# Kernel tuning notes

Hardware: AMD Instinct MI355X
Metric: run time of the kernel (lower is better)

The kernel has to match this reference:

```python
import jax, jax.numpy as jnp
import numpy as np

B, CH, N = 131072, 2, 8  # batch, pos/neg channels, coarse graph size
L1, L2 = 64, 32          # latent_gcn, latent2_gcn
NEG_SLOPE = 0.2


def _row_normalize(a):
    # GCN-style row normalization: D^-1 A, zeroing rows with zero sum
    rowsum = a.sum(-1, keepdims=True)
    r_inv = jnp.where(rowsum > 0, 1.0 / rowsum, 0.0)
    return a * r_inv


def _leaky(x):
    return jnp.where(x >= 0, x, NEG_SLOPE * x)


def setup_inputs() -> dict:
    key = jax.random.key(0)
    ks = jax.random.split(key, 16)
    u = lambda k, shape, s: jax.random.uniform(k, shape, jnp.float32, -s, s)
    s1 = 1.0 / np.sqrt(L1)
    s2 = 1.0 / np.sqrt(L2)
    d_in = CH * N * L2            # 512
    d_h1 = N * N                  # 64
    d_h2 = int(N * N * 0.5)       # 32
    return {
        "adj": jax.random.uniform(ks[0], (B, CH, N, N), jnp.float32),
        "Wp1": u(ks[1], (N, L1), s1),  "bp1": u(ks[2], (L1,), s1),
        "Wp2": u(ks[3], (L1, L2), s2), "bp2": u(ks[4], (L2,), s2),
        "Wn1": u(ks[5], (N, L1), s1),  "bn1": u(ks[6], (L1,), s1),
        "Wn2": u(ks[7], (L1, L2), s2), "bn2": u(ks[8], (L2,), s2),
        "Wl1": u(ks[9], (d_in, d_h1), 1.0 / np.sqrt(d_in)),  "bl1": u(ks[10], (d_h1,), 1.0 / np.sqrt(d_in)),
        "Wl2": u(ks[11], (d_h1, d_h2), 1.0 / np.sqrt(d_h1)), "bl2": u(ks[12], (d_h2,), 1.0 / np.sqrt(d_h1)),
        "Wl3": u(ks[13], (d_h2, 1), 1.0 / np.sqrt(d_h2)),    "bl3": u(ks[14], (1,), 1.0 / np.sqrt(d_h2)),
    }


def reference(adj, Wp1, bp1, Wp2, bp2, Wn1, bn1, Wn2, bn2,
              Wl1, bl1, Wl2, bl2, Wl3, bl3):
    # adj: [B, 2, N, N]; channel 0 -> positive GCN, channel 1 -> negative GCN
    Ap = _row_normalize(adj[:, 0])  # [B, N, N]
    An = _row_normalize(adj[:, 1])

    # input features x = eye(N), so eye @ W == W; keep general via broadcast
    def gcn2(A, W1, b1, W2, b2):
        x1 = _leaky(jnp.einsum('bij,jk->bik', A, W1) + b1)        # [B, N, L1]
        x2 = _leaky(jnp.einsum('bij,bjk->bik', A, x1 @ W2) + b2)  # [B, N, L2]
        return x2

    xp = gcn2(Ap, Wp1, bp1, Wp2, bp2)
    xn = gcn2(An, Wn1, bn1, Wn2, bn2)
    x_ = jnp.stack([xp, xn], axis=1)          # [B, 2, N, L2]
    x = x_.reshape(x_.shape[0], -1)           # [B, 2*N*L2]

    h = _leaky(x @ Wl1 + bl1)
    h = _leaky(h @ Wl2 + bl2)
    return h @ Wl3 + bl3                      # [B, 1]
```

## Files before the change

kernel.cpp:

```cpp
#include <hip/hip_runtime.h>

typedef _Float16 f16;
typedef _Float16 f16x2 __attribute__((ext_vector_type(2)));
typedef _Float16 f16x4 __attribute__((ext_vector_type(4)));
typedef _Float16 f16x8 __attribute__((ext_vector_type(8)));
typedef float    f32x4 __attribute__((ext_vector_type(4)));
typedef unsigned int u32;
typedef u32      u32x2 __attribute__((ext_vector_type(2)));
typedef u32      u32x4 __attribute__((ext_vector_type(4)));

#define MFMA32(a, b, c) __builtin_amdgcn_mfma_f32_16x16x32_f16((a), (b), (c), 0, 0, 0)
#define MFMA16(a, b, c) __builtin_amdgcn_mfma_f32_16x16x16f16((a), (b), (c), 0, 0, 0)

#define TILES 8

__device__ __forceinline__ float leaky(float x) {
    return fmaf(0.4f, __builtin_fabsf(x), 0.6f * x);
}
__device__ __forceinline__ u32 pkrtz(float a, float b) {
    return __builtin_bit_cast(u32, __builtin_amdgcn_cvt_pkrtz(a, b));
}
__device__ __forceinline__ u32 lk_pk2(float a, float b) {
    f16x2 v = __builtin_bit_cast(f16x2, __builtin_amdgcn_cvt_pkrtz(a, b));
    f16x2 z2 = {(f16)0.0f, (f16)0.0f};
    f16x2 mx = __builtin_elementwise_max(v, z2);
    f16x2 mn = __builtin_elementwise_min(v, z2);
    f16x2 r = mn * (f16x2){(f16)0.2f, (f16)0.2f} + mx;
    return __builtin_bit_cast(u32, r);
}
__device__ __forceinline__ f16x4 lk_pk4(const f32x4 z) {
    return __builtin_bit_cast(f16x4, (u32x2){ lk_pk2(z[0], z[1]), lk_pk2(z[2], z[3]) });
}
__device__ __forceinline__ f16x4 pk4(const f32x4 z) {
    return __builtin_bit_cast(f16x4, (u32x2){ pkrtz(z[0], z[1]), pkrtz(z[2], z[3]) });
}
__device__ __forceinline__ void st_lk4(void* p, const f32x4 z) {
    *(u32x2*)p = (u32x2){ lk_pk2(z[0], z[1]), lk_pk2(z[2], z[3]) };
}

__global__ void disc_prepack(const float* __restrict__ Wp1, const float* __restrict__ Wp2,
                             const float* __restrict__ Wn1, const float* __restrict__ Wn2,
                             const float* __restrict__ Wl1, const float* __restrict__ Wl2,
                             f16* __restrict__ ws)
{
    int idx = blockIdx.x * 256 + threadIdx.x;
    if (idx >= 84 * 512 + 24 * 256) return;
    float v = 0.0f;
    if (idx < 84 * 512) {
        int f = idx >> 9, r = idx & 511;
        int lane = r >> 3, e = r & 7;
        int m15 = lane & 15, h = lane >> 4;
        if (f < 64) {
            int mt4 = f >> 4, ks4 = f & 15;
            int k = ks4 * 32 + h * 8 + e;
            v = Wl1[k * 64 + mt4 * 16 + m15];
        } else if (f < 72) {
            int q = f - 64, c = q >> 2, mt = q & 3;
            const float* W1 = c ? Wn1 : Wp1;
            v = (lane < 16) ? W1[e * 64 + mt * 16 + m15] : 0.0f;
        } else if (f < 80) {
            int q = f - 72, c = q >> 2, nt2 = (q >> 1) & 1, ks2 = q & 1;
            const float* W2 = c ? Wn2 : Wp2;
            int k = ks2 * 32 + h * 8 + e;
            v = W2[k * 32 + nt2 * 16 + m15];
        } else {
            int q = f - 80, ms5 = q >> 1, ks5 = q & 1;
            int k = ks5 * 32 + h * 8 + e;
            v = Wl2[k * 32 + ms5 * 16 + m15];
        }
    } else {
        int r2 = idx - 84 * 512;
        int f2 = r2 >> 8, rr = r2 & 255;
        int lane = rr >> 2, e = rr & 3;
        int m15 = lane & 15, h = lane >> 4;
        if (f2 < 16) {
            int c = f2 >> 3, kb = (f2 >> 1) & 3, nt = f2 & 1;
            const float* W2 = c ? Wn2 : Wp2;
            v = W2[(kb * 16 + h * 4 + e) * 32 + nt * 16 + m15];
        } else {
            int q = f2 - 16, kb = q >> 1, nt = q & 1;
            v = Wl2[(kb * 16 + h * 4 + e) * 32 + nt * 16 + m15];
        }
    }
    ws[idx] = (f16)v;
}

__global__ __launch_bounds__(128, 2) void disc_main(
    const float* __restrict__ adj,
    const float* __restrict__ bp1, const float* __restrict__ bp2,
    const float* __restrict__ bn1, const float* __restrict__ bn2,
    const float* __restrict__ bl1, const float* __restrict__ bl2,
    const float* __restrict__ bl3, const float* __restrict__ Wl3,
    const f16* __restrict__ ws, float* __restrict__ out)
{
    extern __shared__ char smem[];
    const int tid  = threadIdx.x;
    const int lane = tid & 63;
    const int wid  = tid >> 6;
    const int h    = lane >> 4;
    const int m15  = lane & 15;
    const int i7   = lane & 7;
    const int r8   = m15 >> 3;

    const f16x8* wsf = (const f16x8*)ws;
    const f16x4* wsq = (const f16x4*)(ws + 84 * 512);
    const int c = wid;

    const f16x8* w1p = wsf + (64 + c * 4) * 64 + lane;
    f16x8 w1t0 = w1p[0], w1t1 = w1p[64], w1t2 = w1p[128], w1t3 = w1p[192];
    const f16x4* w2p = wsq + (c * 8) * 64 + lane;
    f16x4 w2k00 = w2p[0],   w2k01 = w2p[64];
    f16x4 w2k10 = w2p[128], w2k11 = w2p[192];
    f16x4 w2k20 = w2p[256], w2k21 = w2p[320];
    f16x4 w2k30 = w2p[384], w2k31 = w2p[448];
    const f32x4* b1p = (const f32x4*)(c ? bn1 : bp1);
    f32x4 b10 = b1p[h], b11 = b1p[4 + h], b12 = b1p[8 + h], b13 = b1p[12 + h];
    const f32x4* b2p = (const f32x4*)(c ? bn2 : bp2);
    f32x4 b20 = b2p[h], b21 = b2p[4 + h];
    f32x4 bl1v0 = ((const f32x4*)bl1)[h],      bl1v1 = ((const f32x4*)bl1)[4 + h];
    f32x4 bl1v2 = ((const f32x4*)bl1)[8 + h],  bl1v3 = ((const f32x4*)bl1)[12 + h];

    f16x4 l200, l201, l210, l211, l220, l221, l230, l231;
    float c0 = 0.0f, c1 = 0.0f, w30 = 0.0f, w31 = 0.0f, bl3s = 0.0f;
    if (wid == 0) {
        const f16x4* wl2p = wsq + 16 * 64 + lane;
        l200 = wl2p[0];   l201 = wl2p[64];
        l210 = wl2p[128]; l211 = wl2p[192];
        l220 = wl2p[256]; l221 = wl2p[320];
        l230 = wl2p[384]; l231 = wl2p[448];
        c0 = bl2[m15]; c1 = bl2[m15 + 16];
        w30 = Wl3[m15]; w31 = Wl3[m15 + 16];
        bl3s = bl3[0];
    }

    char* wbase = smem + wid * 10240;
    char* Albuf = wbase;
    char* xbuf  = wbase + 2048;

    const int rxor = ((m15 >> 1) & 3) << 4;
    const bool bsel = ((h >> 1) == r8);
    const int  hlow = h & 1;
    f32x4 zero4 = {0.0f, 0.0f, 0.0f, 0.0f};
    f16x4 zf4 = {};

    long b0 = (long)blockIdx.x * (16 * TILES);

    f32x4 c00, c01, c10, c11;
    {
        const f32x4* rp0 = (const f32x4*)(adj + (b0 + (lane >> 3)) * 128 + c * 64 + (lane & 7) * 8);
        c00 = rp0[0]; c01 = rp0[1];
        const int rid1 = 64 + lane;
        const f32x4* rp1 = (const f32x4*)(adj + (b0 + (rid1 >> 3)) * 128 + c * 64 + (rid1 & 7) * 8);
        c10 = rp1[0]; c11 = rp1[1];
    }

    #pragma unroll 1
    for (int it = 0; it < TILES; ++it, b0 += 16) {
        {
            float s = ((c00[0] + c00[1]) + (c00[2] + c00[3])) + ((c01[0] + c01[1]) + (c01[2] + c01[3]));
            float rv = (s > 0.0f) ? __builtin_amdgcn_rcpf(s) : 0.0f;
            u32x4 row = { pkrtz(c00[0] * rv, c00[1] * rv), pkrtz(c00[2] * rv, c00[3] * rv),
                          pkrtz(c01[0] * rv, c01[1] * rv), pkrtz(c01[2] * rv, c01[3] * rv) };
            *(u32x4*)(Albuf + lane * 16) = row;
        }
        {
            float s = ((c10[0] + c10[1]) + (c10[2] + c10[3])) + ((c11[0] + c11[1]) + (c11[2] + c11[3]));
            float rv = (s > 0.0f) ? __builtin_amdgcn_rcpf(s) : 0.0f;
            u32x4 row = { pkrtz(c10[0] * rv, c10[1] * rv), pkrtz(c10[2] * rv, c10[3] * rv),
                          pkrtz(c11[0] * rv, c11[1] * rv), pkrtz(c11[2] * rv, c11[3] * rv) };
            *(u32x4*)(Albuf + (64 + lane) * 16) = row;
        }

        f32x4 n00, n01, n10, n11;
        const bool more = (it + 1 < TILES);
        if (more) {
            const f32x4* rp0 = (const f32x4*)(adj + (b0 + 16 + (lane >> 3)) * 128 + c * 64 + (lane & 7) * 8);
            n00 = rp0[0]; n01 = rp0[1];
            const int rid1 = 64 + lane;
            const f32x4* rp1 = (const f32x4*)(adj + (b0 + 16 + (rid1 >> 3)) * 128 + c * 64 + (rid1 & 7) * 8);
            n10 = rp1[0]; n11 = rp1[1];
        }

        #pragma unroll 2
        for (int tp = 0; tp < 4; ++tp) {
            const int ta = tp, tb = tp + 4;
            f16x8 arow_a = *(const f16x8*)(Albuf + (((2 * ta + r8) * 8 + i7) << 4));
            f16x8 arow_b = *(const f16x8*)(Albuf + (((2 * tb + r8) * 8 + i7) << 4));

            f32x4 z0a = MFMA32(w1t0, arow_a, b10);
            f32x4 z1a = MFMA32(w1t1, arow_a, b11);
            f32x4 z2a = MFMA32(w1t2, arow_a, b12);
            f32x4 z3a = MFMA32(w1t3, arow_a, b13);
            f32x4 z0b = MFMA32(w1t0, arow_b, b10);
            f32x4 z1b = MFMA32(w1t1, arow_b, b11);
            f32x4 z2b = MFMA32(w1t2, arow_b, b12);
            f32x4 z3b = MFMA32(w1t3, arow_b, b13);

            f16x4 xa0 = lk_pk4(z0a), xa1 = lk_pk4(z1a), xa2 = lk_pk4(z2a), xa3 = lk_pk4(z3a);
            f16x4 xb0 = lk_pk4(z0b), xb1 = lk_pk4(z1b), xb2 = lk_pk4(z2b), xb3 = lk_pk4(z3b);

            f32x4 y0a = MFMA16(xa0, w2k00, zero4);
            f32x4 y1a = MFMA16(xa0, w2k01, zero4);
            f32x4 y0b = MFMA16(xb0, w2k00, zero4);
            f32x4 y1b = MFMA16(xb0, w2k01, zero4);
            y0a = MFMA16(xa1, w2k10, y0a);
            y1a = MFMA16(xa1, w2k11, y1a);
            y0b = MFMA16(xb1, w2k10, y0b);
            y1b = MFMA16(xb1, w2k11, y1b);
            y0a = MFMA16(xa2, w2k20, y0a);
            y1a = MFMA16(xa2, w2k21, y1a);
            y0b = MFMA16(xb2, w2k20, y0b);
            y1b = MFMA16(xb2, w2k21, y1b);
            y0a = MFMA16(xa3, w2k30, y0a);
            y1a = MFMA16(xa3, w2k31, y1a);
            y0b = MFMA16(xb3, w2k30, y0b);
            y1b = MFMA16(xb3, w2k31, y1b);

            f16x4 pa0 = pk4(y0a), pa1 = pk4(y1a);
            f16x4 pb0 = pk4(y0b), pb1 = pk4(y1b);
            u32x4 ara = __builtin_bit_cast(u32x4, arow_a);
            u32x4 arb = __builtin_bit_cast(u32x4, arow_b);
            f16x4 halfa = __builtin_bit_cast(f16x4,
                hlow ? (u32x2){ara[2], ara[3]} : (u32x2){ara[0], ara[1]});
            f16x4 halfb = __builtin_bit_cast(f16x4,
                hlow ? (u32x2){arb[2], arb[3]} : (u32x2){arb[0], arb[1]});
            f16x4 bfra = bsel ? halfa : zf4;
            f16x4 bfrb = bsel ? halfb : zf4;

            f32x4 x2aa = MFMA16(pa0, bfra, b20);
            f32x4 x2ba = MFMA16(pa1, bfra, b21);
            f32x4 x2ab = MFMA16(pb0, bfrb, b20);
            f32x4 x2bb = MFMA16(pb1, bfrb, b21);

            const int lga = h >> 1;
            const int lgb = (lga + 2) & 3;
            char* fb = xbuf + (i7 << 10);
            {
                int wx = ((ta & 3) ^ i7) << 4;
                int basew = ((2 * ta + r8) << 6) + ((h & 1) << 3);
                st_lk4(fb + ((basew + lga * 16) ^ wx), x2aa);
                st_lk4(fb + ((basew + lgb * 16) ^ wx), x2ba);
            }
            {
                int wx = ((tb & 3) ^ i7) << 4;
                int basew = ((2 * tb + r8) << 6) + ((h & 1) << 3);
                st_lk4(fb + ((basew + lga * 16) ^ wx), x2ab);
                st_lk4(fb + ((basew + lgb * 16) ^ wx), x2bb);
            }
        }

        f32x4 a40 = wid ? zero4 : bl1v0;
        f32x4 a41 = wid ? zero4 : bl1v1;
        f32x4 a42 = wid ? zero4 : bl1v2;
        f32x4 a43 = wid ? zero4 : bl1v3;
        __builtin_amdgcn_s_setprio(1);
        #pragma unroll 4
        for (int k8 = 0; k8 < 8; ++k8) {
            int xr = rxor ^ (k8 << 4);
            f16x8 xf = *(const f16x8*)(xbuf + (k8 << 10) + ((m15 * 64 + h * 16) ^ xr));
            const f16x8* wl = wsf + (c * 8 + k8) * 64 + lane;
            a40 = MFMA32(wl[0],    xf, a40);
            a41 = MFMA32(wl[1024], xf, a41);
            a42 = MFMA32(wl[2048], xf, a42);
            a43 = MFMA32(wl[3072], xf, a43);
        }
        __builtin_amdgcn_s_setprio(0);

        char* xc = smem + 20480 + ((it & 1) << 12);
        if (wid == 1) {
            *(f32x4*)(xc +    0 + lane * 16) = a40;
            *(f32x4*)(xc + 1024 + lane * 16) = a41;
            *(f32x4*)(xc + 2048 + lane * 16) = a42;
            *(f32x4*)(xc + 3072 + lane * 16) = a43;
        }
        __syncthreads();

        if (wid == 0) {
            a40 += *(const f32x4*)(xc +    0 + lane * 16);
            a41 += *(const f32x4*)(xc + 1024 + lane * 16);
            a42 += *(const f32x4*)(xc + 2048 + lane * 16);
            a43 += *(const f32x4*)(xc + 3072 + lane * 16);

            f16x4 pd0 = lk_pk4(a40), pd1 = lk_pk4(a41);
            f16x4 pd2 = lk_pk4(a42), pd3 = lk_pk4(a43);

            f32x4 a50 = {c0, c0, c0, c0};
            f32x4 a51 = {c1, c1, c1, c1};
            a50 = MFMA16(pd0, l200, a50);
            a51 = MFMA16(pd0, l201, a51);
            a50 = MFMA16(pd1, l210, a50);
            a51 = MFMA16(pd1, l211, a51);
            a50 = MFMA16(pd2, l220, a50);
            a51 = MFMA16(pd2, l221, a51);
            a50 = MFMA16(pd3, l230, a50);
            a51 = MFMA16(pd3, l231, a51);

            #pragma unroll
            for (int r = 0; r < 4; ++r) {
                float acc = leaky(a50[r]) * w30 + leaky(a51[r]) * w31;
                acc += __shfl_xor(acc, 1);
                acc += __shfl_xor(acc, 2);
                acc += __shfl_xor(acc, 4);
                acc += __shfl_xor(acc, 8);
                if (m15 == 0) out[b0 + h * 4 + r] = acc + bl3s;
            }
        }

        if (more) { c00 = n00; c01 = n01; c10 = n10; c11 = n11; }
    }
}

extern "C" void kernel_launch(void* const* d_in, const int* in_sizes, int n_in,
                              void* d_out, int out_size, void* d_ws, size_t ws_size,
                              hipStream_t stream)
{
    const float* adj  = (const float*)d_in[0];
    const float* Wp1  = (const float*)d_in[1];
    const float* bp1  = (const float*)d_in[2];
    const float* Wp2  = (const float*)d_in[3];
    const float* bp2  = (const float*)d_in[4];
    const float* Wn1  = (const float*)d_in[5];
    const float* bn1  = (const float*)d_in[6];
    const float* Wn2  = (const float*)d_in[7];
    const float* bn2  = (const float*)d_in[8];
    const float* Wl1  = (const float*)d_in[9];
    const float* bl1  = (const float*)d_in[10];
    const float* Wl2  = (const float*)d_in[11];
    const float* bl2  = (const float*)d_in[12];
    const float* Wl3  = (const float*)d_in[13];
    const float* bl3  = (const float*)d_in[14];
    f16* ws = (f16*)d_ws;
    float* out = (float*)d_out;

    hipLaunchKernelGGL(disc_prepack, dim3(192), dim3(256), 0, stream,
                       Wp1, Wp2, Wn1, Wn2, Wl1, Wl2, ws);

    const int ldsBytes = 28672;
    hipFuncSetAttribute(reinterpret_cast<const void*>(disc_main),
                        hipFuncAttributeMaxDynamicSharedMemorySize, ldsBytes);
    hipLaunchKernelGGL(disc_main, dim3(8192 / TILES), dim3(128), ldsBytes, stream,
                       adj, bp1, bp2, bn1, bn2, bl1, bl2, bl3, Wl3, ws, out);
}
```

Baseline: 53.62 us.

## Keep half of Wl1 weights in registers and split accumulators for layer-1 MFMA chain

Result: slower. 92.22 us (+72.0%).

```diff
diff --git a/kernel.cpp b/kernel.cpp
--- a/kernel.cpp
+++ b/kernel.cpp
@@ -22,10 +22,8 @@
 }
 __device__ __forceinline__ u32 lk_pk2(float a, float b) {
     f16x2 v = __builtin_bit_cast(f16x2, __builtin_amdgcn_cvt_pkrtz(a, b));
-    f16x2 z2 = {(f16)0.0f, (f16)0.0f};
-    f16x2 mx = __builtin_elementwise_max(v, z2);
-    f16x2 mn = __builtin_elementwise_min(v, z2);
-    f16x2 r = mn * (f16x2){(f16)0.2f, (f16)0.2f} + mx;
+    f16x2 s = v * (f16x2){(f16)0.2f, (f16)0.2f};
+    f16x2 r = __builtin_elementwise_max(v, s);
     return __builtin_bit_cast(u32, r);
 }
 __device__ __forceinline__ f16x4 lk_pk4(const f32x4 z) {
@@ -120,6 +118,16 @@
     f32x4 bl1v0 = ((const f32x4*)bl1)[h],      bl1v1 = ((const f32x4*)bl1)[4 + h];
     f32x4 bl1v2 = ((const f32x4*)bl1)[8 + h],  bl1v3 = ((const f32x4*)bl1)[12 + h];
 
+    f16x8 wr[16];
+    #pragma unroll
+    for (int k8 = 0; k8 < 4; ++k8) {
+        const f16x8* wl = wsf + (c * 8 + k8) * 64 + lane;
+        wr[4 * k8 + 0] = wl[0];
+        wr[4 * k8 + 1] = wl[1024];
+        wr[4 * k8 + 2] = wl[2048];
+        wr[4 * k8 + 3] = wl[3072];
+    }
+
     f16x4 l200, l201, l210, l211, l220, l221, l230, l231;
     float c0 = 0.0f, c1 = 0.0f, w30 = 0.0f, w31 = 0.0f, bl3s = 0.0f;
     if (wid == 0) {
@@ -181,7 +189,7 @@
             n10 = rp1[0]; n11 = rp1[1];
         }
 
-        #pragma unroll 2
+        #pragma unroll 1
         for (int tp = 0; tp < 4; ++tp) {
             const int ta = tp, tb = tp + 4;
             f16x8 arow_a = *(const f16x8*)(Albuf + (((2 * ta + r8) * 8 + i7) << 4));
@@ -253,18 +261,28 @@
         f32x4 a41 = wid ? zero4 : bl1v1;
         f32x4 a42 = wid ? zero4 : bl1v2;
         f32x4 a43 = wid ? zero4 : bl1v3;
+        f32x4 b40 = zero4, b41 = zero4, b42 = zero4, b43 = zero4;
         __builtin_amdgcn_s_setprio(1);
-        #pragma unroll 4
-        for (int k8 = 0; k8 < 8; ++k8) {
-            int xr = rxor ^ (k8 << 4);
-            f16x8 xf = *(const f16x8*)(xbuf + (k8 << 10) + ((m15 * 64 + h * 16) ^ xr));
-            const f16x8* wl = wsf + (c * 8 + k8) * 64 + lane;
-            a40 = MFMA32(wl[0],    xf, a40);
-            a41 = MFMA32(wl[1024], xf, a41);
-            a42 = MFMA32(wl[2048], xf, a42);
-            a43 = MFMA32(wl[3072], xf, a43);
+        #pragma unroll
+        for (int j = 0; j < 4; ++j) {
+            const int kv = 4 + j;
+            const f16x8* wl = wsf + (c * 8 + kv) * 64 + lane;
+            f16x8 wv0 = wl[0], wv1 = wl[1024], wv2 = wl[2048], wv3 = wl[3072];
+            int xrv = rxor ^ (kv << 4);
+            f16x8 xfv = *(const f16x8*)(xbuf + (kv << 10) + ((m15 * 64 + h * 16) ^ xrv));
+            int xr = rxor ^ (j << 4);
+            f16x8 xf = *(const f16x8*)(xbuf + (j << 10) + ((m15 * 64 + h * 16) ^ xr));
+            a40 = MFMA32(wr[4 * j + 0], xf, a40);
+            a41 = MFMA32(wr[4 * j + 1], xf, a41);
+            a42 = MFMA32(wr[4 * j + 2], xf, a42);
+            a43 = MFMA32(wr[4 * j + 3], xf, a43);
+            b40 = MFMA32(wv0, xfv, b40);
+            b41 = MFMA32(wv1, xfv, b41);
+            b42 = MFMA32(wv2, xfv, b42);
+            b43 = MFMA32(wv3, xfv, b43);
         }
         __builtin_amdgcn_s_setprio(0);
+        a40 += b40; a41 += b41; a42 += b42; a43 += b43;
 
         char* xc = smem + 20480 + ((it & 1) << 12);
         if (wid == 1) {
```

## Process two tiles per dense-layer pass to reuse Wl1 fragment loads

Applied to the files above, without the earlier changes.

Result: slower. 71.83 us (+34.0%).

```diff
diff --git a/kernel.cpp b/kernel.cpp
--- a/kernel.cpp
+++ b/kernel.cpp
@@ -22,10 +22,8 @@
 }
 __device__ __forceinline__ u32 lk_pk2(float a, float b) {
     f16x2 v = __builtin_bit_cast(f16x2, __builtin_amdgcn_cvt_pkrtz(a, b));
-    f16x2 z2 = {(f16)0.0f, (f16)0.0f};
-    f16x2 mx = __builtin_elementwise_max(v, z2);
-    f16x2 mn = __builtin_elementwise_min(v, z2);
-    f16x2 r = mn * (f16x2){(f16)0.2f, (f16)0.2f} + mx;
+    f16x2 s = v * (f16x2){(f16)0.2f, (f16)0.2f};
+    f16x2 r = __builtin_elementwise_max(v, s);
     return __builtin_bit_cast(u32, r);
 }
 __device__ __forceinline__ f16x4 lk_pk4(const f32x4 z) {
@@ -133,7 +131,7 @@
         bl3s = bl3[0];
     }
 
-    char* wbase = smem + wid * 10240;
+    char* wbase = smem + wid * 18432;
     char* Albuf = wbase;
     char* xbuf  = wbase + 2048;
 
@@ -143,109 +141,115 @@
     f32x4 zero4 = {0.0f, 0.0f, 0.0f, 0.0f};
     f16x4 zf4 = {};
 
-    long b0 = (long)blockIdx.x * (16 * TILES);
+    const long blockBase = (long)blockIdx.x * (16 * TILES);
 
     f32x4 c00, c01, c10, c11;
     {
-        const f32x4* rp0 = (const f32x4*)(adj + (b0 + (lane >> 3)) * 128 + c * 64 + (lane & 7) * 8);
+        const f32x4* rp0 = (const f32x4*)(adj + (blockBase + (lane >> 3)) * 128 + c * 64 + (lane & 7) * 8);
         c00 = rp0[0]; c01 = rp0[1];
         const int rid1 = 64 + lane;
-        const f32x4* rp1 = (const f32x4*)(adj + (b0 + (rid1 >> 3)) * 128 + c * 64 + (rid1 & 7) * 8);
+        const f32x4* rp1 = (const f32x4*)(adj + (blockBase + (rid1 >> 3)) * 128 + c * 64 + (rid1 & 7) * 8);
         c10 = rp1[0]; c11 = rp1[1];
     }
 
     #pragma unroll 1
-    for (int it = 0; it < TILES; ++it, b0 += 16) {
-        {
-            float s = ((c00[0] + c00[1]) + (c00[2] + c00[3])) + ((c01[0] + c01[1]) + (c01[2] + c01[3]));
-            float rv = (s > 0.0f) ? __builtin_amdgcn_rcpf(s) : 0.0f;
-            u32x4 row = { pkrtz(c00[0] * rv, c00[1] * rv), pkrtz(c00[2] * rv, c00[3] * rv),
-                          pkrtz(c01[0] * rv, c01[1] * rv), pkrtz(c01[2] * rv, c01[3] * rv) };
-            *(u32x4*)(Albuf + lane * 16) = row;
-        }
-        {
-            float s = ((c10[0] + c10[1]) + (c10[2] + c10[3])) + ((c11[0] + c11[1]) + (c11[2] + c11[3]));
-            float rv = (s > 0.0f) ? __builtin_amdgcn_rcpf(s) : 0.0f;
-            u32x4 row = { pkrtz(c10[0] * rv, c10[1] * rv), pkrtz(c10[2] * rv, c10[3] * rv),
-                          pkrtz(c11[0] * rv, c11[1] * rv), pkrtz(c11[2] * rv, c11[3] * rv) };
-            *(u32x4*)(Albuf + (64 + lane) * 16) = row;
-        }
-
-        f32x4 n00, n01, n10, n11;
-        const bool more = (it + 1 < TILES);
-        if (more) {
-            const f32x4* rp0 = (const f32x4*)(adj + (b0 + 16 + (lane >> 3)) * 128 + c * 64 + (lane & 7) * 8);
-            n00 = rp0[0]; n01 = rp0[1];
-            const int rid1 = 64 + lane;
-            const f32x4* rp1 = (const f32x4*)(adj + (b0 + 16 + (rid1 >> 3)) * 128 + c * 64 + (rid1 & 7) * 8);
-            n10 = rp1[0]; n11 = rp1[1];
-        }
-
-        #pragma unroll 2
-        for (int tp = 0; tp < 4; ++tp) {
-            const int ta = tp, tb = tp + 4;
-            f16x8 arow_a = *(const f16x8*)(Albuf + (((2 * ta + r8) * 8 + i7) << 4));
-            f16x8 arow_b = *(const f16x8*)(Albuf + (((2 * tb + r8) * 8 + i7) << 4));
-
-            f32x4 z0a = MFMA32(w1t0, arow_a, b10);
-            f32x4 z1a = MFMA32(w1t1, arow_a, b11);
-            f32x4 z2a = MFMA32(w1t2, arow_a, b12);
-            f32x4 z3a = MFMA32(w1t3, arow_a, b13);
-            f32x4 z0b = MFMA32(w1t0, arow_b, b10);
-            f32x4 z1b = MFMA32(w1t1, arow_b, b11);
-            f32x4 z2b = MFMA32(w1t2, arow_b, b12);
-            f32x4 z3b = MFMA32(w1t3, arow_b, b13);
-
-            f16x4 xa0 = lk_pk4(z0a), xa1 = lk_pk4(z1a), xa2 = lk_pk4(z2a), xa3 = lk_pk4(z3a);
-            f16x4 xb0 = lk_pk4(z0b), xb1 = lk_pk4(z1b), xb2 = lk_pk4(z2b), xb3 = lk_pk4(z3b);
-
-            f32x4 y0a = MFMA16(xa0, w2k00, zero4);
-            f32x4 y1a = MFMA16(xa0, w2k01, zero4);
-            f32x4 y0b = MFMA16(xb0, w2k00, zero4);
-            f32x4 y1b = MFMA16(xb0, w2k01, zero4);
-            y0a = MFMA16(xa1, w2k10, y0a);
-            y1a = MFMA16(xa1, w2k11, y1a);
-            y0b = MFMA16(xb1, w2k10, y0b);
-            y1b = MFMA16(xb1, w2k11, y1b);
-            y0a = MFMA16(xa2, w2k20, y0a);
-            y1a = MFMA16(xa2, w2k21, y1a);
-            y0b = MFMA16(xb2, w2k20, y0b);
-            y1b = MFMA16(xb2, w2k21, y1b);
-            y0a = MFMA16(xa3, w2k30, y0a);
-            y1a = MFMA16(xa3, w2k31, y1a);
-            y0b = MFMA16(xb3, w2k30, y0b);
-            y1b = MFMA16(xb3, w2k31, y1b);
-
-            f16x4 pa0 = pk4(y0a), pa1 = pk4(y1a);
-            f16x4 pb0 = pk4(y0b), pb1 = pk4(y1b);
-            u32x4 ara = __builtin_bit_cast(u32x4, arow_a);
-            u32x4 arb = __builtin_bit_cast(u32x4, arow_b);
-            f16x4 halfa = __builtin_bit_cast(f16x4,
-                hlow ? (u32x2){ara[2], ara[3]} : (u32x2){ara[0], ara[1]});
-            f16x4 halfb = __builtin_bit_cast(f16x4,
-                hlow ? (u32x2){arb[2], arb[3]} : (u32x2){arb[0], arb[1]});
-            f16x4 bfra = bsel ? halfa : zf4;
-            f16x4 bfrb = bsel ? halfb : zf4;
-
-            f32x4 x2aa = MFMA16(pa0, bfra, b20);
-            f32x4 x2ba = MFMA16(pa1, bfra, b21);
-            f32x4 x2ab = MFMA16(pb0, bfrb, b20);
-            f32x4 x2bb = MFMA16(pb1, bfrb, b21);
-
-            const int lga = h >> 1;
-            const int lgb = (lga + 2) & 3;
-            char* fb = xbuf + (i7 << 10);
+    for (int itp = 0; itp < TILES / 2; ++itp) {
+        #pragma unroll 1
+        for (int sub = 0; sub < 2; ++sub) {
+            const int  itile = itp * 2 + sub;
+            const long tb    = blockBase + (long)itile * 16;
+
             {
-                int wx = ((ta & 3) ^ i7) << 4;
-                int basew = ((2 * ta + r8) << 6) + ((h & 1) << 3);
-                st_lk4(fb + ((basew + lga * 16) ^ wx), x2aa);
-                st_lk4(fb + ((basew + lgb * 16) ^ wx), x2ba);
+                float s = ((c00[0] + c00[1]) + (c00[2] + c00[3])) + ((c01[0] + c01[1]) + (c01[2] + c01[3]));
+                float rv = (s > 0.0f) ? __builtin_amdgcn_rcpf(s) : 0.0f;
+                u32x4 row = { pkrtz(c00[0] * rv, c00[1] * rv), pkrtz(c00[2] * rv, c00[3] * rv),
+                              pkrtz(c01[0] * rv, c01[1] * rv), pkrtz(c01[2] * rv, c01[3] * rv) };
+                *(u32x4*)(Albuf + lane * 16) = row;
             }
             {
-                int wx = ((tb & 3) ^ i7) << 4;
-                int basew = ((2 * tb + r8) << 6) + ((h & 1) << 3);
-                st_lk4(fb + ((basew + lga * 16) ^ wx), x2ab);
-                st_lk4(fb + ((basew + lgb * 16) ^ wx), x2bb);
+                float s = ((c10[0] + c10[1]) + (c10[2] + c10[3])) + ((c11[0] + c11[1]) + (c11[2] + c11[3]));
+                float rv = (s > 0.0f) ? __builtin_amdgcn_rcpf(s) : 0.0f;
+                u32x4 row = { pkrtz(c10[0] * rv, c10[1] * rv), pkrtz(c10[2] * rv, c10[3] * rv),
+                              pkrtz(c11[0] * rv, c11[1] * rv), pkrtz(c11[2] * rv, c11[3] * rv) };
+                *(u32x4*)(Albuf + (64 + lane) * 16) = row;
+            }
+
+            if (itile < TILES - 1) {
+                const long nb = tb + 16;
+                const f32x4* rp0 = (const f32x4*)(adj + (nb + (lane >> 3)) * 128 + c * 64 + (lane & 7) * 8);
+                c00 = rp0[0]; c01 = rp0[1];
+                const int rid1 = 64 + lane;
+                const f32x4* rp1 = (const f32x4*)(adj + (nb + (rid1 >> 3)) * 128 + c * 64 + (rid1 & 7) * 8);
+                c10 = rp1[0]; c11 = rp1[1];
+            }
+
+            char* xsub = xbuf + (sub << 13);
+            #pragma unroll 2
+            for (int tp = 0; tp < 4; ++tp) {
+                const int ta = tp, tbn = tp + 4;
+                f16x8 arow_a = *(const f16x8*)(Albuf + (((2 * ta + r8) * 8 + i7) << 4));
+                f16x8 arow_b = *(const f16x8*)(Albuf + (((2 * tbn + r8) * 8 + i7) << 4));
+
+                f32x4 z0a = MFMA32(w1t0, arow_a, b10);
+                f32x4 z1a = MFMA32(w1t1, arow_a, b11);
+                f32x4 z2a = MFMA32(w1t2, arow_a, b12);
+                f32x4 z3a = MFMA32(w1t3, arow_a, b13);
+                f32x4 z0b = MFMA32(w1t0, arow_b, b10);
+                f32x4 z1b = MFMA32(w1t1, arow_b, b11);
+                f32x4 z2b = MFMA32(w1t2, arow_b, b12);
+                f32x4 z3b = MFMA32(w1t3, arow_b, b13);
+
+                f16x4 xa0 = lk_pk4(z0a), xa1 = lk_pk4(z1a), xa2 = lk_pk4(z2a), xa3 = lk_pk4(z3a);
+                f16x4 xb0 = lk_pk4(z0b), xb1 = lk_pk4(z1b), xb2 = lk_pk4(z2b), xb3 = lk_pk4(z3b);
+
+                f32x4 y0a = MFMA16(xa0, w2k00, zero4);
+                f32x4 y1a = MFMA16(xa0, w2k01, zero4);
+                f32x4 y0b = MFMA16(xb0, w2k00, zero4);
+                f32x4 y1b = MFMA16(xb0, w2k01, zero4);
+                y0a = MFMA16(xa1, w2k10, y0a);
+                y1a = MFMA16(xa1, w2k11, y1a);
+                y0b = MFMA16(xb1, w2k10, y0b);
+                y1b = MFMA16(xb1, w2k11, y1b);
+                y0a = MFMA16(xa2, w2k20, y0a);
+                y1a = MFMA16(xa2, w2k21, y1a);
+                y0b = MFMA16(xb2, w2k20, y0b);
+                y1b = MFMA16(xb2, w2k21, y1b);
+                y0a = MFMA16(xa3, w2k30, y0a);
+                y1a = MFMA16(xa3, w2k31, y1a);
+                y0b = MFMA16(xb3, w2k30, y0b);
+                y1b = MFMA16(xb3, w2k31, y1b);
+
+                f16x4 pa0 = pk4(y0a), pa1 = pk4(y1a);
+                f16x4 pb0 = pk4(y0b), pb1 = pk4(y1b);
+                u32x4 ara = __builtin_bit_cast(u32x4, arow_a);
+                u32x4 arb = __builtin_bit_cast(u32x4, arow_b);
+                f16x4 halfa = __builtin_bit_cast(f16x4,
+                    hlow ? (u32x2){ara[2], ara[3]} : (u32x2){ara[0], ara[1]});
+                f16x4 halfb = __builtin_bit_cast(f16x4,
+                    hlow ? (u32x2){arb[2], arb[3]} : (u32x2){arb[0], arb[1]});
+                f16x4 bfra = bsel ? halfa : zf4;
+                f16x4 bfrb = bsel ? halfb : zf4;
+
+                f32x4 x2aa = MFMA16(pa0, bfra, b20);
+                f32x4 x2ba = MFMA16(pa1, bfra, b21);
+                f32x4 x2ab = MFMA16(pb0, bfrb, b20);
+                f32x4 x2bb = MFMA16(pb1, bfrb, b21);
+
+                const int lga = h >> 1;
+                const int lgb = (lga + 2) & 3;
+                char* fb = xsub + (i7 << 10);
+                {
+                    int wx = ((ta & 3) ^ i7) << 4;
+                    int basew = ((2 * ta + r8) << 6) + ((h & 1) << 3);
+                    st_lk4(fb + ((basew + lga * 16) ^ wx), x2aa);
+                    st_lk4(fb + ((basew + lgb * 16) ^ wx), x2ba);
+                }
+                {
+                    int wx = ((tbn & 3) ^ i7) << 4;
+                    int basew = ((2 * tbn + r8) << 6) + ((h & 1) << 3);
+                    st_lk4(fb + ((basew + lga * 16) ^ wx), x2ab);
+                    st_lk4(fb + ((basew + lgb * 16) ^ wx), x2bb);
+                }
             }
         }
 
@@ -253,60 +257,100 @@
         f32x4 a41 = wid ? zero4 : bl1v1;
         f32x4 a42 = wid ? zero4 : bl1v2;
         f32x4 a43 = wid ? zero4 : bl1v3;
+        f32x4 e40 = wid ? zero4 : bl1v0;
+        f32x4 e41 = wid ? zero4 : bl1v1;
+        f32x4 e42 = wid ? zero4 : bl1v2;
+        f32x4 e43 = wid ? zero4 : bl1v3;
         __builtin_amdgcn_s_setprio(1);
         #pragma unroll 4
         for (int k8 = 0; k8 < 8; ++k8) {
-            int xr = rxor ^ (k8 << 4);
-            f16x8 xf = *(const f16x8*)(xbuf + (k8 << 10) + ((m15 * 64 + h * 16) ^ xr));
             const f16x8* wl = wsf + (c * 8 + k8) * 64 + lane;
-            a40 = MFMA32(wl[0],    xf, a40);
-            a41 = MFMA32(wl[1024], xf, a41);
-            a42 = MFMA32(wl[2048], xf, a42);
-            a43 = MFMA32(wl[3072], xf, a43);
+            f16x8 w0 = wl[0], w1 = wl[1024], w2 = wl[2048], w3 = wl[3072];
+            int xoff = (k8 << 10) + ((m15 * 64 + h * 16) ^ (rxor ^ (k8 << 4)));
+            f16x8 xfa = *(const f16x8*)(xbuf + xoff);
+            f16x8 xfb = *(const f16x8*)(xbuf + 8192 + xoff);
+            a40 = MFMA32(w0, xfa, a40);
+            e40 = MFMA32(w0, xfb, e40);
+            a41 = MFMA32(w1, xfa, a41);
+            e41 = MFMA32(w1, xfb, e41);
+            a42 = MFMA32(w2, xfa, a42);
+            e42 = MFMA32(w2, xfb, e42);
+            a43 = MFMA32(w3, xfa, a43);
+            e43 = MFMA32(w3, xfb, e43);
         }
         __builtin_amdgcn_s_setprio(0);
 
-        char* xc = smem + 20480 + ((it & 1) << 12);
+        char* xc = smem + 36864 + ((itp & 1) << 13);
         if (wid == 1) {
             *(f32x4*)(xc +    0 + lane * 16) = a40;
             *(f32x4*)(xc + 1024 + lane * 16) = a41;
             *(f32x4*)(xc + 2048 + lane * 16) = a42;
             *(f32x4*)(xc + 3072 + lane * 16) = a43;
+            *(f32x4*)(xc + 4096 + lane * 16) = e40;
+            *(f32x4*)(xc + 5120 + lane * 16) = e41;
+            *(f32x4*)(xc + 6144 + lane * 16) = e42;
+            *(f32x4*)(xc + 7168 + lane * 16) = e43;
         }
         __syncthreads();
 
         if (wid == 0) {
+            const long ob = blockBase + (long)itp * 32;
             a40 += *(const f32x4*)(xc +    0 + lane * 16);
             a41 += *(const f32x4*)(xc + 1024 + lane * 16);
             a42 += *(const f32x4*)(xc + 2048 + lane * 16);
             a43 += *(const f32x4*)(xc + 3072 + lane * 16);
-
-            f16x4 pd0 = lk_pk4(a40), pd1 = lk_pk4(a41);
-            f16x4 pd2 = lk_pk4(a42), pd3 = lk_pk4(a43);
-
-            f32x4 a50 = {c0, c0, c0, c0};
-            f32x4 a51 = {c1, c1, c1, c1};
-            a50 = MFMA16(pd0, l200, a50);
-            a51 = MFMA16(pd0, l201, a51);
-            a50 = MFMA16(pd1, l210, a50);
-            a51 = MFMA16(pd1, l211, a51);
-            a50 = MFMA16(pd2, l220, a50);
-            a51 = MFMA16(pd2, l221, a51);
-            a50 = MFMA16(pd3, l230, a50);
-            a51 = MFMA16(pd3, l231, a51);
-
-            #pragma unroll
-            for (int r = 0; r < 4; ++r) {
-                float acc = leaky(a50[r]) * w30 + leaky(a51[r]) * w31;
-                acc += __shfl_xor(acc, 1);
-                acc += __shfl_xor(acc, 2);
-                acc += __shfl_xor(acc, 4);
-                acc += __shfl_xor(acc, 8);
-                if (m15 == 0) out[b0 + h * 4 + r] = acc + bl3s;
-            }
-        }
-
-        if (more) { c00 = n00; c01 = n01; c10 = n10; c11 = n11; }
+            e40 += *(const f32x4*)(xc + 4096 + lane * 16);
+            e41 += *(const f32x4*)(xc + 5120 + lane * 16);
+            e42 += *(const f32x4*)(xc + 6144 + lane * 16);
+            e43 += *(const f32x4*)(xc + 7168 + lane * 16);
+
+            {
+                f16x4 pd0 = lk_pk4(a40), pd1 = lk_pk4(a41);
+                f16x4 pd2 = lk_pk4(a42), pd3 = lk_pk4(a43);
+                f32x4 a50 = {c0, c0, c0, c0};
+                f32x4 a51 = {c1, c1, c1, c1};
+                a50 = MFMA16(pd0, l200, a50);
+                a51 = MFMA16(pd0, l201, a51);
+                a50 = MFMA16(pd1, l210, a50);
+                a51 = MFMA16(pd1, l211, a51);
+                a50 = MFMA16(pd2, l220, a50);
+                a51 = MFMA16(pd2, l221, a51);
+                a50 = MFMA16(pd3, l230, a50);
+                a51 = MFMA16(pd3, l231, a51);
+                #pragma unroll
+                for (int r = 0; r < 4; ++r) {
+                    float acc = leaky(a50[r]) * w30 + leaky(a51[r]) * w31;
+                    acc += __shfl_xor(acc, 1);
+                    acc += __shfl_xor(acc, 2);
+                    acc += __shfl_xor(acc, 4);
+                    acc += __shfl_xor(acc, 8);
+                    if (m15 == 0) out[ob + h * 4 + r] = acc + bl3s;
+                }
+            }
+            {
+                f16x4 pd0 = lk_pk4(e40), pd1 = lk_pk4(e41);
+                f16x4 pd2 = lk_pk4(e42), pd3 = lk_pk4(e43);
+                f32x4 a50 = {c0, c0, c0, c0};
+                f32x4 a51 = {c1, c1, c1, c1};
+                a50 = MFMA16(pd0, l200, a50);
+                a51 = MFMA16(pd0, l201, a51);
+                a50 = MFMA16(pd1, l210, a50);
+                a51 = MFMA16(pd1, l211, a51);
+                a50 = MFMA16(pd2, l220, a50);
+                a51 = MFMA16(pd2, l221, a51);
+                a50 = MFMA16(pd3, l230, a50);
+                a51 = MFMA16(pd3, l231, a51);
+                #pragma unroll
+                for (int r = 0; r < 4; ++r) {
+                    float acc = leaky(a50[r]) * w30 + leaky(a51[r]) * w31;
+                    acc += __shfl_xor(acc, 1);
+                    acc += __shfl_xor(acc, 2);
+                    acc += __shfl_xor(acc, 4);
+                    acc += __shfl_xor(acc, 8);
+                    if (m15 == 0) out[ob + 16 + h * 4 + r] = acc + bl3s;
+                }
+            }
+        }
     }
 }
 
@@ -335,7 +379,7 @@
     hipLaunchKernelGGL(disc_prepack, dim3(192), dim3(256), 0, stream,
                        Wp1, Wp2, Wn1, Wn2, Wl1, Wl2, ws);
 
-    const int ldsBytes = 28672;
+    const int ldsBytes = 53248;
     hipFuncSetAttribute(reinterpret_cast<const void*>(disc_main),
                         hipFuncAttributeMaxDynamicSharedMemorySize, ldsBytes);
     hipLaunchKernelGGL(disc_main, dim3(8192 / TILES), dim3(128), ldsBytes, stream,
```

## Software-pipeline GCN stage with Wl1 MLP stage using double-buffered feature tiles

Applied to the files above, without the earlier changes.

New measurement: 56.96 us. 6.2% more time.

```diff
diff --git a/kernel.cpp b/kernel.cpp
--- a/kernel.cpp
+++ b/kernel.cpp
@@ -12,7 +12,7 @@
 #define MFMA32(a, b, c) __builtin_amdgcn_mfma_f32_16x16x32_f16((a), (b), (c), 0, 0, 0)
 #define MFMA16(a, b, c) __builtin_amdgcn_mfma_f32_16x16x16f16((a), (b), (c), 0, 0, 0)
 
-#define TILES 8
+#define TILES 4
 
 __device__ __forceinline__ float leaky(float x) {
     return fmaf(0.4f, __builtin_fabsf(x), 0.6f * x);
@@ -22,10 +22,8 @@
 }
 __device__ __forceinline__ u32 lk_pk2(float a, float b) {
     f16x2 v = __builtin_bit_cast(f16x2, __builtin_amdgcn_cvt_pkrtz(a, b));
-    f16x2 z2 = {(f16)0.0f, (f16)0.0f};
-    f16x2 mx = __builtin_elementwise_max(v, z2);
-    f16x2 mn = __builtin_elementwise_min(v, z2);
-    f16x2 r = mn * (f16x2){(f16)0.2f, (f16)0.2f} + mx;
+    f16x2 s = v * (f16x2){(f16)0.2f, (f16)0.2f};
+    f16x2 r = __builtin_elementwise_max(v, s);
     return __builtin_bit_cast(u32, r);
 }
 __device__ __forceinline__ f16x4 lk_pk4(const f32x4 z) {
@@ -133,9 +131,10 @@
         bl3s = bl3[0];
     }
 
-    char* wbase = smem + wid * 10240;
+    char* wbase = smem + wid * 18432;
     char* Albuf = wbase;
-    char* xbuf  = wbase + 2048;
+    char* xb0   = wbase + 2048;
+    char* xb1   = wbase + 2048 + 8192;
 
     const int rxor = ((m15 >> 1) & 3) << 4;
     const bool bsel = ((h >> 1) == r8);
@@ -143,19 +142,19 @@
     f32x4 zero4 = {0.0f, 0.0f, 0.0f, 0.0f};
     f16x4 zf4 = {};
 
-    long b0 = (long)blockIdx.x * (16 * TILES);
+    const long blockBase = (long)blockIdx.x * (16 * TILES);
 
     f32x4 c00, c01, c10, c11;
-    {
-        const f32x4* rp0 = (const f32x4*)(adj + (b0 + (lane >> 3)) * 128 + c * 64 + (lane & 7) * 8);
+    f32x4 a40, a41, a42, a43;
+
+    auto doPF = [&](long tb) {
+        const f32x4* rp0 = (const f32x4*)(adj + (tb + (lane >> 3)) * 128 + c * 64 + (lane & 7) * 8);
         c00 = rp0[0]; c01 = rp0[1];
         const int rid1 = 64 + lane;
-        const f32x4* rp1 = (const f32x4*)(adj + (b0 + (rid1 >> 3)) * 128 + c * 64 + (rid1 & 7) * 8);
+        const f32x4* rp1 = (const f32x4*)(adj + (tb + (rid1 >> 3)) * 128 + c * 64 + (rid1 & 7) * 8);
         c10 = rp1[0]; c11 = rp1[1];
-    }
-
-    #pragma unroll 1
-    for (int it = 0; it < TILES; ++it, b0 += 16) {
+    };
+    auto doA = [&]() {
         {
             float s = ((c00[0] + c00[1]) + (c00[2] + c00[3])) + ((c01[0] + c01[1]) + (c01[2] + c01[3]));
             float rv = (s > 0.0f) ? __builtin_amdgcn_rcpf(s) : 0.0f;
@@ -170,103 +169,98 @@
                           pkrtz(c11[0] * rv, c11[1] * rv), pkrtz(c11[2] * rv, c11[3] * rv) };
             *(u32x4*)(Albuf + (64 + lane) * 16) = row;
         }
-
-        f32x4 n00, n01, n10, n11;
-        const bool more = (it + 1 < TILES);
-        if (more) {
-            const f32x4* rp0 = (const f32x4*)(adj + (b0 + 16 + (lane >> 3)) * 128 + c * 64 + (lane & 7) * 8);
-            n00 = rp0[0]; n01 = rp0[1];
-            const int rid1 = 64 + lane;
-            const f32x4* rp1 = (const f32x4*)(adj + (b0 + 16 + (rid1 >> 3)) * 128 + c * 64 + (rid1 & 7) * 8);
-            n10 = rp1[0]; n11 = rp1[1];
-        }
-
-        #pragma unroll 2
-        for (int tp = 0; tp < 4; ++tp) {
-            const int ta = tp, tb = tp + 4;
-            f16x8 arow_a = *(const f16x8*)(Albuf + (((2 * ta + r8) * 8 + i7) << 4));
-            f16x8 arow_b = *(const f16x8*)(Albuf + (((2 * tb + r8) * 8 + i7) << 4));
-
-            f32x4 z0a = MFMA32(w1t0, arow_a, b10);
-            f32x4 z1a = MFMA32(w1t1, arow_a, b11);
-            f32x4 z2a = MFMA32(w1t2, arow_a, b12);
-            f32x4 z3a = MFMA32(w1t3, arow_a, b13);
-            f32x4 z0b = MFMA32(w1t0, arow_b, b10);
-            f32x4 z1b = MFMA32(w1t1, arow_b, b11);
-            f32x4 z2b = MFMA32(w1t2, arow_b, b12);
-            f32x4 z3b = MFMA32(w1t3, arow_b, b13);
-
-            f16x4 xa0 = lk_pk4(z0a), xa1 = lk_pk4(z1a), xa2 = lk_pk4(z2a), xa3 = lk_pk4(z3a);
-            f16x4 xb0 = lk_pk4(z0b), xb1 = lk_pk4(z1b), xb2 = lk_pk4(z2b), xb3 = lk_pk4(z3b);
-
-            f32x4 y0a = MFMA16(xa0, w2k00, zero4);
-            f32x4 y1a = MFMA16(xa0, w2k01, zero4);
-            f32x4 y0b = MFMA16(xb0, w2k00, zero4);
-            f32x4 y1b = MFMA16(xb0, w2k01, zero4);
-            y0a = MFMA16(xa1, w2k10, y0a);
-            y1a = MFMA16(xa1, w2k11, y1a);
-            y0b = MFMA16(xb1, w2k10, y0b);
-            y1b = MFMA16(xb1, w2k11, y1b);
-            y0a = MFMA16(xa2, w2k20, y0a);
-            y1a = MFMA16(xa2, w2k21, y1a);
-            y0b = MFMA16(xb2, w2k20, y0b);
-            y1b = MFMA16(xb2, w2k21, y1b);
-            y0a = MFMA16(xa3, w2k30, y0a);
-            y1a = MFMA16(xa3, w2k31, y1a);
-            y0b = MFMA16(xb3, w2k30, y0b);
-            y1b = MFMA16(xb3, w2k31, y1b);
-
-            f16x4 pa0 = pk4(y0a), pa1 = pk4(y1a);
-            f16x4 pb0 = pk4(y0b), pb1 = pk4(y1b);
-            u32x4 ara = __builtin_bit_cast(u32x4, arow_a);
-            u32x4 arb = __builtin_bit_cast(u32x4, arow_b);
-            f16x4 halfa = __builtin_bit_cast(f16x4,
-                hlow ? (u32x2){ara[2], ara[3]} : (u32x2){ara[0], ara[1]});
-            f16x4 halfb = __builtin_bit_cast(f16x4,
-                hlow ? (u32x2){arb[2], arb[3]} : (u32x2){arb[0], arb[1]});
-            f16x4 bfra = bsel ? halfa : zf4;
-            f16x4 bfrb = bsel ? halfb : zf4;
-
-            f32x4 x2aa = MFMA16(pa0, bfra, b20);
-            f32x4 x2ba = MFMA16(pa1, bfra, b21);
-            f32x4 x2ab = MFMA16(pb0, bfrb, b20);
-            f32x4 x2bb = MFMA16(pb1, bfrb, b21);
-
-            const int lga = h >> 1;
-            const int lgb = (lga + 2) & 3;
-            char* fb = xbuf + (i7 << 10);
-            {
-                int wx = ((ta & 3) ^ i7) << 4;
-                int basew = ((2 * ta + r8) << 6) + ((h & 1) << 3);
-                st_lk4(fb + ((basew + lga * 16) ^ wx), x2aa);
-                st_lk4(fb + ((basew + lgb * 16) ^ wx), x2ba);
-            }
-            {
-                int wx = ((tb & 3) ^ i7) << 4;
-                int basew = ((2 * tb + r8) << 6) + ((h & 1) << 3);
-                st_lk4(fb + ((basew + lga * 16) ^ wx), x2ab);
-                st_lk4(fb + ((basew + lgb * 16) ^ wx), x2bb);
-            }
-        }
-
-        f32x4 a40 = wid ? zero4 : bl1v0;
-        f32x4 a41 = wid ? zero4 : bl1v1;
-        f32x4 a42 = wid ? zero4 : bl1v2;
-        f32x4 a43 = wid ? zero4 : bl1v3;
-        __builtin_amdgcn_s_setprio(1);
-        #pragma unroll 4
-        for (int k8 = 0; k8 < 8; ++k8) {
-            int xr = rxor ^ (k8 << 4);
-            f16x8 xf = *(const f16x8*)(xbuf + (k8 << 10) + ((m15 * 64 + h * 16) ^ xr));
+    };
+    auto seed = [&]() {
+        a40 = wid ? zero4 : bl1v0;
+        a41 = wid ? zero4 : bl1v1;
+        a42 = wid ? zero4 : bl1v2;
+        a43 = wid ? zero4 : bl1v3;
+    };
+
+    auto phaseB = [&](int tp, char* xsub) {
+        const int ta = tp, tbn = tp + 4;
+        f16x8 arow_a = *(const f16x8*)(Albuf + (((2 * ta + r8) * 8 + i7) << 4));
+        f16x8 arow_b = *(const f16x8*)(Albuf + (((2 * tbn + r8) * 8 + i7) << 4));
+
+        f32x4 z0a = MFMA32(w1t0, arow_a, b10);
+        f32x4 z1a = MFMA32(w1t1, arow_a, b11);
+        f32x4 z2a = MFMA32(w1t2, arow_a, b12);
+        f32x4 z3a = MFMA32(w1t3, arow_a, b13);
+        f32x4 z0b = MFMA32(w1t0, arow_b, b10);
+        f32x4 z1b = MFMA32(w1t1, arow_b, b11);
+        f32x4 z2b = MFMA32(w1t2, arow_b, b12);
+        f32x4 z3b = MFMA32(w1t3, arow_b, b13);
+
+        f16x4 xa0 = lk_pk4(z0a), xa1 = lk_pk4(z1a), xa2 = lk_pk4(z2a), xa3 = lk_pk4(z3a);
+        f16x4 xb0v = lk_pk4(z0b), xb1v = lk_pk4(z1b), xb2v = lk_pk4(z2b), xb3v = lk_pk4(z3b);
+
+        f32x4 y0a = MFMA16(xa0, w2k00, zero4);
+        f32x4 y1a = MFMA16(xa0, w2k01, zero4);
+        f32x4 y0b = MFMA16(xb0v, w2k00, zero4);
+        f32x4 y1b = MFMA16(xb0v, w2k01, zero4);
+        y0a = MFMA16(xa1, w2k10, y0a);
+        y1a = MFMA16(xa1, w2k11, y1a);
+        y0b = MFMA16(xb1v, w2k10, y0b);
+        y1b = MFMA16(xb1v, w2k11, y1b);
+        y0a = MFMA16(xa2, w2k20, y0a);
+        y1a = MFMA16(xa2, w2k21, y1a);
+        y0b = MFMA16(xb2v, w2k20, y0b);
+        y1b = MFMA16(xb2v, w2k21, y1b);
+        y0a = MFMA16(xa3, w2k30, y0a);
+        y1a = MFMA16(xa3, w2k31, y1a);
+        y0b = MFMA16(xb3v, w2k30, y0b);
+        y1b = MFMA16(xb3v, w2k31, y1b);
+
+        f16x4 pa0 = pk4(y0a), pa1 = pk4(y1a);
+        f16x4 pb0 = pk4(y0b), pb1 = pk4(y1b);
+        u32x4 ara = __builtin_bit_cast(u32x4, arow_a);
+        u32x4 arb = __builtin_bit_cast(u32x4, arow_b);
+        f16x4 halfa = __builtin_bit_cast(f16x4,
+            hlow ? (u32x2){ara[2], ara[3]} : (u32x2){ara[0], ara[1]});
+        f16x4 halfb = __builtin_bit_cast(f16x4,
+            hlow ? (u32x2){arb[2], arb[3]} : (u32x2){arb[0], arb[1]});
+        f16x4 bfra = bsel ? halfa : zf4;
+        f16x4 bfrb = bsel ? halfb : zf4;
+
+        f32x4 x2aa = MFMA16(pa0, bfra, b20);
+        f32x4 x2ba = MFMA16(pa1, bfra, b21);
+        f32x4 x2ab = MFMA16(pb0, bfrb, b20);
+        f32x4 x2bb = MFMA16(pb1, bfrb, b21);
+
+        const int lga = h >> 1;
+        const int lgb = (lga + 2) & 3;
+        char* fb = xsub + (i7 << 10);
+        {
+            int wx = ((ta & 3) ^ i7) << 4;
+            int basew = ((2 * ta + r8) << 6) + ((h & 1) << 3);
+            st_lk4(fb + ((basew + lga * 16) ^ wx), x2aa);
+            st_lk4(fb + ((basew + lgb * 16) ^ wx), x2ba);
+        }
+        {
+            int wx = ((tbn & 3) ^ i7) << 4;
+            int basew = ((2 * tbn + r8) << 6) + ((h & 1) << 3);
+            st_lk4(fb + ((basew + lga * 16) ^ wx), x2ab);
+            st_lk4(fb + ((basew + lgb * 16) ^ wx), x2bb);
+        }
+    };
+
+    auto phaseC2 = [&](int k8a, char* xprev) {
+        #pragma unroll
+        for (int u = 0; u < 2; ++u) {
+            const int k8 = k8a + u;
             const f16x8* wl = wsf + (c * 8 + k8) * 64 + lane;
-            a40 = MFMA32(wl[0],    xf, a40);
-            a41 = MFMA32(wl[1024], xf, a41);
-            a42 = MFMA32(wl[2048], xf, a42);
-            a43 = MFMA32(wl[3072], xf, a43);
-        }
-        __builtin_amdgcn_s_setprio(0);
-
-        char* xc = smem + 20480 + ((it & 1) << 12);
+            f16x8 w0 = wl[0], w1 = wl[1024], w2 = wl[2048], w3 = wl[3072];
+            int xoff = (k8 << 10) + ((m15 * 64 + h * 16) ^ (rxor ^ (k8 << 4)));
+            f16x8 xf = *(const f16x8*)(xprev + xoff);
+            a40 = MFMA32(w0, xf, a40);
+            a41 = MFMA32(w1, xf, a41);
+            a42 = MFMA32(w2, xf, a42);
+            a43 = MFMA32(w3, xf, a43);
+        }
+    };
+
+    auto exchTail = [&](int jt) {
+        char* xc = smem + 18432 + 2048 + ((jt & 1) << 13);
         if (wid == 1) {
             *(f32x4*)(xc +    0 + lane * 16) = a40;
             *(f32x4*)(xc + 1024 + lane * 16) = a41;
@@ -274,16 +268,18 @@
             *(f32x4*)(xc + 3072 + lane * 16) = a43;
         }
         __syncthreads();
-
+        f32x4 p0, p1, p2, p3;
         if (wid == 0) {
-            a40 += *(const f32x4*)(xc +    0 + lane * 16);
-            a41 += *(const f32x4*)(xc + 1024 + lane * 16);
-            a42 += *(const f32x4*)(xc + 2048 + lane * 16);
-            a43 += *(const f32x4*)(xc + 3072 + lane * 16);
-
+            p0 = *(const f32x4*)(xc +    0 + lane * 16);
+            p1 = *(const f32x4*)(xc + 1024 + lane * 16);
+            p2 = *(const f32x4*)(xc + 2048 + lane * 16);
+            p3 = *(const f32x4*)(xc + 3072 + lane * 16);
+        }
+        __syncthreads();
+        if (wid == 0) {
+            a40 += p0; a41 += p1; a42 += p2; a43 += p3;
             f16x4 pd0 = lk_pk4(a40), pd1 = lk_pk4(a41);
             f16x4 pd2 = lk_pk4(a42), pd3 = lk_pk4(a43);
-
             f32x4 a50 = {c0, c0, c0, c0};
             f32x4 a51 = {c1, c1, c1, c1};
             a50 = MFMA16(pd0, l200, a50);
@@ -294,7 +290,7 @@
             a51 = MFMA16(pd2, l221, a51);
             a50 = MFMA16(pd3, l230, a50);
             a51 = MFMA16(pd3, l231, a51);
-
+            const long ob = blockBase + (long)jt * 16;
             #pragma unroll
             for (int r = 0; r < 4; ++r) {
                 float acc = leaky(a50[r]) * w30 + leaky(a51[r]) * w31;
@@ -302,12 +298,50 @@
                 acc += __shfl_xor(acc, 2);
                 acc += __shfl_xor(acc, 4);
                 acc += __shfl_xor(acc, 8);
-                if (m15 == 0) out[b0 + h * 4 + r] = acc + bl3s;
+                if (m15 == 0) out[ob + h * 4 + r] = acc + bl3s;
             }
         }
-
-        if (more) { c00 = n00; c01 = n01; c10 = n10; c11 = n11; }
+    };
+
+    doPF(blockBase);
+    doA();
+    doPF(blockBase + 16);
+    seed();
+
+    #pragma unroll 1
+    for (int tp = 0; tp < 4; ++tp) phaseB(tp, xb0);
+    doA();
+    doPF(blockBase + 32);
+
+    #pragma unroll 1
+    for (int it = 1; it < TILES; ++it) {
+        char* xcur  = (it & 1) ? xb1 : xb0;
+        char* xprev = (it & 1) ? xb0 : xb1;
+        __builtin_amdgcn_s_setprio(1);
+        #pragma unroll 1
+        for (int tp = 0; tp < 4; ++tp) {
+            phaseC2(2 * tp, xprev);
+            phaseB(tp, xcur);
+        }
+        __builtin_amdgcn_s_setprio(0);
+        exchTail(it - 1);
+        seed();
+        if (it + 1 < TILES) {
+            doA();
+            if (it + 2 < TILES) doPF(blockBase + (long)(it + 2) * 16);
+        }
     }
+
+    {
+        char* xprev = ((TILES - 1) & 1) ? xb1 : xb0;
+        __builtin_amdgcn_s_setprio(1);
+        phaseC2(0, xprev);
+        phaseC2(2, xprev);
+        phaseC2(4, xprev);
+        phaseC2(6, xprev);
+        __builtin_amdgcn_s_setprio(0);
+    }
+    exchTail(TILES - 1);
 }
 
 extern "C" void kernel_launch(void* const* d_in, const int* in_sizes, int n_in,
@@ -335,7 +369,7 @@
     hipLaunchKernelGGL(disc_prepack, dim3(192), dim3(256), 0, stream,
                        Wp1, Wp2, Wn1, Wn2, Wl1, Wl2, ws);
 
-    const int ldsBytes = 28672;
+    const int ldsBytes = 36864;
     hipFuncSetAttribute(reinterpret_cast<const void*>(disc_main),
                         hipFuncAttributeMaxDynamicSharedMemorySize, ldsBytes);
     hipLaunchKernelGGL(disc_main, dim3(8192 / TILES), dim3(128), ldsBytes, stream,
```
